# Optimization experiments

Measured on AMD Instinct MI355X. Metric: run time of the kernel, lower is better.

## Reference

```python
import jax, jax.numpy as jnp
import numpy as np

N, E, IN, H, OUT, L = 20000, 320000, 256, 256, 128, 3
EPS = 1e-5


def setup_inputs() -> dict:
    key = jax.random.key(0)
    ks = jax.random.split(key, 16)
    s = 0.02
    return {
        "x": jax.random.normal(ks[0], (N, IN), jnp.float32),
        "edge_index": jax.random.randint(ks[1], (2, E), 0, N, jnp.int64),
        "in_w": jax.random.normal(ks[2], (IN, H), jnp.float32) * s,
        "in_b": jnp.zeros((H,), jnp.float32),
        "parent_w": jax.random.normal(ks[3], (L, H, H), jnp.float32) * s,
        "child_w": jax.random.normal(ks[4], (L, H, H), jnp.float32) * s,
        "self_w": jax.random.normal(ks[5], (L, H, H), jnp.float32) * s,
        "self_b": jnp.zeros((L, H), jnp.float32),
        "ln_g": jnp.ones((L, H), jnp.float32),
        "ln_b": jnp.zeros((L, H), jnp.float32),
        "head_w1": jax.random.normal(ks[6], (H, H), jnp.float32) * s,
        "head_b1": jnp.zeros((H,), jnp.float32),
        "head_w2": jax.random.normal(ks[7], (H, OUT), jnp.float32) * s,
        "head_b2": jnp.zeros((OUT,), jnp.float32),
    }


def _aggregate(h, src, dst, weight):
    # gather -> matmul -> scatter-add -> degree-normalize
    transformed = h[src] @ weight                       # [E, H]
    agg = jax.ops.segment_sum(transformed, dst, num_segments=N)
    deg = jax.ops.segment_sum(jnp.ones((src.shape[0],), h.dtype), dst, num_segments=N)
    deg = jnp.maximum(deg, 1.0)
    return agg / deg[:, None]


def _layer_norm(x, g, b):
    mu = jnp.mean(x, axis=-1, keepdims=True)
    var = jnp.mean(jnp.square(x - mu), axis=-1, keepdims=True)
    return (x - mu) * jax.lax.rsqrt(var + EPS) * g + b


def reference(x, edge_index, in_w, in_b, parent_w, child_w, self_w, self_b,
              ln_g, ln_b, head_w1, head_b1, head_w2, head_b2):
    src, dst = edge_index[0], edge_index[1]
    h = x @ in_w + in_b                                  # input_proj
    for l in range(L):
        parent_msg = _aggregate(h, src, dst, parent_w[l])
        child_msg = _aggregate(h, dst, src, child_w[l])  # reversed edges
        out = h @ self_w[l] + self_b[l] + parent_msg + child_msg
        out = jax.nn.gelu(out, approximate=False)
        # dropout is identity in eval mode (training=False)
        h = _layer_norm(h + out, ln_g[l], ln_b[l])
    y = jax.nn.gelu(h @ head_w1 + head_b1, approximate=False)
    return y @ head_w2 + head_b2
```

## Files before the change

### kernel.cpp

```cpp
#include <hip/hip_runtime.h>


#define H 256
#define LAYERS 3
#define OUTD 128
#define LN_EPS 1e-5f

typedef short s16x8 __attribute__((ext_vector_type(8)));
typedef unsigned short u16x4 __attribute__((ext_vector_type(4)));
typedef unsigned short u16x8 __attribute__((ext_vector_type(8)));
typedef float f32x4 __attribute__((ext_vector_type(4)));
typedef int i32x4 __attribute__((ext_vector_type(4)));

__device__ __forceinline__ unsigned short f2bf(float f) {
  unsigned int u = __float_as_uint(f);
  u += 0x7FFFu + ((u >> 16) & 1u);
  return (unsigned short)(u >> 16);
}
__device__ __forceinline__ float bf2f(unsigned short s) {
  return __uint_as_float(((unsigned int)s) << 16);
}
__device__ __forceinline__ float gelu_f(float x) {
  return 0.5f * x * (1.0f + erff(x * 0.70710678118654752440f));
}
__device__ __forceinline__ void gload16(const void* g, void* l) {
  __builtin_amdgcn_global_load_lds((const __attribute__((address_space(1))) void*)g,
                                   (__attribute__((address_space(3))) void*)l, 16, 0, 0);
}


__device__ __forceinline__ void store_split8(unsigned short* __restrict__ T, int NS, int sec,
                                             int row, int l, u16x4 hv, u16x4 lv) {
  size_t tb = ((size_t)((row >> 4) * NS + sec) << 4) + (l >> 3);
  int off = (((row & 15) + (((l >> 1) & 3) << 4)) << 3) + ((l & 1) << 2);
  *(u16x4*)(T + tb * 512 + off) = hv;
  *(u16x4*)(T + (tb + 8) * 512 + off) = lv;
}

__global__ void split_tiles_kernel(const float* __restrict__ X,
                                   unsigned short* __restrict__ T, int NS, int sec,
                                   unsigned short* __restrict__ Hc, int M)
{
  const int rb = blockIdx.x;
  const int l = threadIdx.x & 63;
  const int cq = threadIdx.x >> 6;
  const int row = (rb << 4) + (l & 15);
  if (row >= M) return;
  const float* xr = X + (size_t)row * H;
#pragma unroll
  for (int p = 0; p < 2; ++p) {
    const int c = cq + (p << 2);
    const int j0 = (c << 5) + ((l >> 4) << 3);
    f32x4 v0 = *(const f32x4*)(xr + j0);
    f32x4 v1 = *(const f32x4*)(xr + j0 + 4);
    u16x8 hv, lv;
#pragma unroll
    for (int i = 0; i < 4; ++i) {
      unsigned short hb = f2bf(v0[i]); hv[i] = hb;     lv[i] = f2bf(v0[i] - bf2f(hb));
      unsigned short hc = f2bf(v1[i]); hv[4 + i] = hc; lv[4 + i] = f2bf(v1[i] - bf2f(hc));
    }
    size_t tb = ((size_t)(rb * NS + sec) << 4);
    *(u16x8*)(T + (tb + c) * 512 + (l << 3)) = hv;
    *(u16x8*)(T + (tb + c + 8) * 512 + (l << 3)) = lv;
    if (Hc) *(u16x8*)(Hc + (size_t)row * H + j0) = hv;
  }
}

__global__ void bext_kernel(const float* __restrict__ W, unsigned short* __restrict__ Bt, int ncol) {
  int idx = blockIdx.x * 256 + threadIdx.x;
  if (idx >= H * ncol) return;
  int k = idx / ncol;
  int n = idx - k * ncol;
  float w = W[idx];
  unsigned short hb = f2bf(w);
  unsigned short lb = f2bf(w - bf2f(hb));
  size_t base = (((size_t)(n >> 4) << 4) + (k >> 5)) * 512 +
                (((n & 15) + (((k >> 3) & 3) << 4)) << 3) + (k & 7);
  Bt[base] = hb;
  Bt[base + 8 * 512] = lb;
}

__global__ void zero2_kernel(int* __restrict__ a, int* __restrict__ b, int n) {
  int i = blockIdx.x * 256 + threadIdx.x;
  if (i < n) { a[i] = 0; b[i] = 0; }
}

__global__ void deg_kernel(const int* __restrict__ src, const int* __restrict__ dst,
                           int* __restrict__ di, int* __restrict__ dox, int E) {
  int e = blockIdx.x * 256 + threadIdx.x;
  if (e >= E) return;
  atomicAdd(&dox[src[e]], 1);
  atomicAdd(&di[dst[e]], 1);
}

__global__ void rdeg_kernel(const int* __restrict__ di, const int* __restrict__ dox,
                            float* __restrict__ ri, float* __restrict__ ro, int n) {
  int i = blockIdx.x * 256 + threadIdx.x;
  if (i >= n) return;
  int a = di[i];  if (a < 1) a = 1;
  int b = dox[i]; if (b < 1) b = 1;
  ri[i] = 1.0f / (float)a;
  ro[i] = 1.0f / (float)b;
}

__global__ __launch_bounds__(1024)
void scan_kernel(const int* __restrict__ deg, int* __restrict__ rowptr, int n) {
  __shared__ int partial[1024];
  const int t = threadIdx.x;
  const int chunk = (n + 1023) / 1024;
  int b = t * chunk;
  int e = b + chunk; if (e > n) e = n;
  int s = 0;
  for (int i = b; i < e; ++i) s += deg[i];
  partial[t] = s;
  __syncthreads();
  for (int off = 1; off < 1024; off <<= 1) {
    int v = (t >= off) ? partial[t - off] : 0;
    __syncthreads();
    partial[t] += v;
    __syncthreads();
  }
  int run = (t == 0) ? 0 : partial[t - 1];
  for (int i = b; i < e; ++i) { rowptr[i] = run; run += deg[i]; }
  if (t == 1023) rowptr[n] = run;
}

__global__ void fill_kernel(const int* __restrict__ src, const int* __restrict__ dst,
                            const int* __restrict__ rp_in, const int* __restrict__ rp_out,
                            int* __restrict__ cur_in, int* __restrict__ cur_out,
                            int* __restrict__ ci_in, int* __restrict__ ci_out, int E) {
  int e = blockIdx.x * 256 + threadIdx.x;
  if (e >= E) return;
  int s = src[e], d = dst[e];
  int p = atomicAdd(&cur_in[d], 1);
  ci_in[rp_in[d] + p] = s;
  int q = atomicAdd(&cur_out[s], 1);
  ci_out[rp_out[s] + q] = d;
}

template<int NF>
__global__ __launch_bounds__(256)
void gemm_kernel(const unsigned short* __restrict__ A, int NSa,
                 const unsigned short* __restrict__ B0,
                 const unsigned short* __restrict__ B1,
                 const unsigned short* __restrict__ B2,
                 const float* __restrict__ bias, float* __restrict__ C,
                 int M, int nrb, int nsec, int do_gelu)
{
  constexpr int N = NF * 64;
  constexpr int NBT = N / 16;
  constexpr int BITER = NBT / 4;
  constexpr int SA_HI = 0, SA_LO = 2048, SB_HI = 4096;
  constexpr int SB_LO = 4096 + NBT * 512;
  __shared__ unsigned short lds[2][4096 + 2 * NBT * 512];

  const int tid = threadIdx.x;
  const int lane = tid & 63;
  const int wn = tid >> 6;
  const int m0 = blockIdx.x << 6;
  int rbw = (blockIdx.x << 2) + wn;
  if (rbw >= nrb) rbw = nrb - 1;

  f32x4 acc[4][NF] = {};

  auto STAGE = [&](int buf, int step) {
    const int s = step >> 3;
    const int c = step & 7;
    const unsigned short* Bs = (s == 0) ? B0 : ((s == 1) ? B1 : B2);
    unsigned short* base = &lds[buf][0];
    const unsigned short* pa = A + (((size_t)(rbw * NSa + s) << 4) + c) * 512 + (lane << 3);
    gload16(pa,        base + SA_HI + (wn << 9));
    gload16(pa + 4096, base + SA_LO + (wn << 9));
#pragma unroll
    for (int i = 0; i < BITER; ++i) {
      const int nb = wn + (i << 2);
      const unsigned short* pb = Bs + (((size_t)nb << 4) + c) * 512 + (lane << 3);
      gload16(pb,        base + SB_HI + (nb << 9));
      gload16(pb + 4096, base + SB_LO + (nb << 9));
    }
  };

  auto COMPUTE = [&](int buf) {
    const unsigned short* base = &lds[buf][0];
    s16x8 ah[4], al[4], bh[NF], bl[NF];
#pragma unroll
    for (int f = 0; f < 4; ++f) {
      ah[f] = *(const s16x8*)(base + SA_HI + (f << 9) + (lane << 3));
      al[f] = *(const s16x8*)(base + SA_LO + (f << 9) + (lane << 3));
    }
#pragma unroll
    for (int j = 0; j < NF; ++j) {
      const int g = wn * NF + j;
      bh[j] = *(const s16x8*)(base + SB_HI + (g << 9) + (lane << 3));
      bl[j] = *(const s16x8*)(base + SB_LO + (g << 9) + (lane << 3));
    }
#pragma unroll
    for (int i = 0; i < 4; ++i)
#pragma unroll
      for (int j = 0; j < NF; ++j)
        acc[i][j] = __builtin_amdgcn_mfma_f32_16x16x32_bf16(ah[i], bh[j], acc[i][j], 0, 0, 0);
#pragma unroll
    for (int i = 0; i < 4; ++i)
#pragma unroll
      for (int j = 0; j < NF; ++j)
        acc[i][j] = __builtin_amdgcn_mfma_f32_16x16x32_bf16(ah[i], bl[j], acc[i][j], 0, 0, 0);
#pragma unroll
    for (int i = 0; i < 4; ++i)
#pragma unroll
      for (int j = 0; j < NF; ++j)
        acc[i][j] = __builtin_amdgcn_mfma_f32_16x16x32_bf16(al[i], bh[j], acc[i][j], 0, 0, 0);
  };

  const int nsteps = nsec << 3;
  STAGE(0, 0);
  int cur = 0;
  for (int t = 0; t < nsteps - 1; ++t) {
    STAGE(cur ^ 1, t + 1);
    if (NF == 4) asm volatile("s_waitcnt vmcnt(10)" ::: "memory");
    else         asm volatile("s_waitcnt vmcnt(6)"  ::: "memory");
    __builtin_amdgcn_s_barrier();
    COMPUTE(cur);
    asm volatile("s_waitcnt lgkmcnt(0)" ::: "memory");
    __builtin_amdgcn_s_barrier();
    cur ^= 1;
  }
  asm volatile("s_waitcnt vmcnt(0)" ::: "memory");
  __builtin_amdgcn_s_barrier();
  COMPUTE(cur);

  const int r0 = (lane >> 4) << 2;
  const int cn = lane & 15;
#pragma unroll
  for (int j = 0; j < NF; ++j) {
    const int col = wn * (NF << 4) + (j << 4) + cn;
    const float bb = bias ? bias[col] : 0.0f;
#pragma unroll
    for (int i = 0; i < 4; ++i) {
      const int rowb = m0 + (i << 4) + r0;
#pragma unroll
      for (int r = 0; r < 4; ++r) {
        const int rr = rowb + r;
        if (rr < M) {
          float v = acc[i][j][r] + bb;
          if (do_gelu) v = gelu_f(v);
          C[(size_t)rr * N + col] = v;
        }
      }
    }
  }
}

__device__ __forceinline__ void gacc8(const int* __restrict__ ci, int beg, int end,
                                      const unsigned short* __restrict__ Hc, int foff,
                                      float* __restrict__ acc) {
  int i = beg;
  for (; i < end && (i & 3); ++i) {
    u16x8 a = *(const u16x8*)(Hc + ((size_t)ci[i] << 8) + foff);
#pragma unroll
    for (int z = 0; z < 8; ++z) acc[z] += bf2f(a[z]);
  }
  for (; i + 4 <= end; i += 4) {
    i32x4 id = *(const i32x4*)(ci + i);
    u16x8 a = *(const u16x8*)(Hc + ((size_t)id[0] << 8) + foff);
    u16x8 b = *(const u16x8*)(Hc + ((size_t)id[1] << 8) + foff);
    u16x8 c = *(const u16x8*)(Hc + ((size_t)id[2] << 8) + foff);
    u16x8 d = *(const u16x8*)(Hc + ((size_t)id[3] << 8) + foff);
#pragma unroll
    for (int z = 0; z < 8; ++z)
      acc[z] += (bf2f(a[z]) + bf2f(b[z])) + (bf2f(c[z]) + bf2f(d[z]));
  }
  for (; i < end; ++i) {
    u16x8 a = *(const u16x8*)(Hc + ((size_t)ci[i] << 8) + foff);
#pragma unroll
    for (int z = 0; z < 8; ++z) acc[z] += bf2f(a[z]);
  }
}

__global__ __launch_bounds__(256)
void gather_kernel(
    const int* __restrict__ rp_in, const int* __restrict__ ci_in,
    const int* __restrict__ rp_out, const int* __restrict__ ci_out,
    const float* __restrict__ ri, const float* __restrict__ ro,
    const unsigned short* __restrict__ Hc, unsigned short* __restrict__ Aext,
    int M, int nrb, int npair)
{
  __shared__ unsigned short sh[2][2][2][2][512];
  const int b = blockIdx.x;
  const int xcd = b & 7;
  const int s = xcd >> 1;
  const int rbp = ((b >> 3) << 1) + (xcd & 1);
  if (rbp >= npair) return;
  const int tid = threadIdx.x;
  const int g = tid >> 3;
  const int t = tid & 7;
  const int row = (rbp << 5) + g;
  const int foff = (s << 6) + (t << 3);

  float hin[8] = {}, hout[8] = {};
  float wi = 0.f, wo = 0.f;
  if (row < M) {
    gacc8(ci_in,  rp_in[row],  rp_in[row + 1],  Hc, foff, hin);
    gacc8(ci_out, rp_out[row], rp_out[row + 1], Hc, foff, hout);
    wi = ri[row];
    wo = ro[row];
  }

  const int rbl = g >> 4;
  const int cc = t >> 2;
  const int pos = ((g & 15) << 3) + ((t & 3) << 7);
  u16x8 hv, lv;
#pragma unroll
  for (int q = 0; q < 8; ++q) {
    float v = hin[q] * wi;
    unsigned short hb = f2bf(v);
    hv[q] = hb; lv[q] = f2bf(v - bf2f(hb));
  }
  *(u16x8*)(&sh[rbl][0][0][cc][pos]) = hv;
  *(u16x8*)(&sh[rbl][0][1][cc][pos]) = lv;
#pragma unroll
  for (int q = 0; q < 8; ++q) {
    float v = hout[q] * wo;
    unsigned short hb = f2bf(v);
    hv[q] = hb; lv[q] = f2bf(v - bf2f(hb));
  }
  *(u16x8*)(&sh[rbl][1][0][cc][pos]) = hv;
  *(u16x8*)(&sh[rbl][1][1][cc][pos]) = lv;
  __syncthreads();

  const int tp = tid >> 4;
  const int q = tid & 15;
  const int rbl2 = tp >> 3, sec = (tp >> 2) & 1, hilo = (tp >> 1) & 1, c2 = tp & 1;
  const int rb = (rbp << 1) + rbl2;
  if (rb < nrb) {
    const int cg = (s << 1) + c2 + (hilo << 3);
    size_t tile = ((size_t)(rb * 3 + 1 + sec) << 4) + cg;
    unsigned short* dstp = Aext + tile * 512;
    const unsigned short* srcp = &sh[rbl2][sec][hilo][c2][0];
#pragma unroll
    for (int i = 0; i < 4; ++i)
      *(u16x8*)(dstp + (i << 7) + (q << 3)) = *(const u16x8*)(srcp + (i << 7) + (q << 3));
  }
}

__global__ void finalize_kernel(float* __restrict__ h, const float* __restrict__ P,
                                unsigned short* __restrict__ Aext,
                                unsigned short* __restrict__ Hc,
                                const float* __restrict__ g, const float* __restrict__ b, int M)
{
  int row = blockIdx.x * 4 + (threadIdx.x >> 6);
  if (row >= M) return;
  int l = threadIdx.x & 63;
  int j = l << 2;
  f32x4 hv = *(const f32x4*)(h + (size_t)row * H + j);
  f32x4 pv = *(const f32x4*)(P + (size_t)row * H + j);
  f32x4 t;
  float sum = 0.f, sq = 0.f;
#pragma unroll
  for (int i = 0; i < 4; ++i) {
    t[i] = hv[i] + gelu_f(pv[i]);
    sum += t[i];
    sq += t[i] * t[i];
  }
#pragma unroll
  for (int off = 1; off < 64; off <<= 1) {
    sum += __shfl_xor(sum, off, 64);
    sq  += __shfl_xor(sq, off, 64);
  }
  float mu = sum * (1.0f / H);
  float var = sq * (1.0f / H) - mu * mu;
  float rs = rsqrtf(var + LN_EPS);
  f32x4 outv;
  u16x4 hvv, lvv;
#pragma unroll
  for (int i = 0; i < 4; ++i) {
    outv[i] = (t[i] - mu) * rs * g[j + i] + b[j + i];
    unsigned short hb = f2bf(outv[i]);
    hvv[i] = hb;
    lvv[i] = f2bf(outv[i] - bf2f(hb));
  }
  *(f32x4*)(h + (size_t)row * H + j) = outv;
  *(u16x4*)(Hc + ((size_t)row << 8) + j) = hvv;
  store_split8(Aext, 3, 0, row, l, hvv, lvv);
}

extern "C" void kernel_launch(void* const* d_in, const int* in_sizes, int n_in,
                              void* d_out, int out_size, void* d_ws, size_t ws_size,
                              hipStream_t stream)
{
  const float* x        = (const float*)d_in[0];
  const int*   ei       = (const int*)d_in[1];
  const float* in_w     = (const float*)d_in[2];
  const float* in_b     = (const float*)d_in[3];
  const float* parent_w = (const float*)d_in[4];
  const float* child_w  = (const float*)d_in[5];
  const float* self_w   = (const float*)d_in[6];
  const float* self_b   = (const float*)d_in[7];
  const float* ln_g     = (const float*)d_in[8];
  const float* ln_b     = (const float*)d_in[9];
  const float* head_w1  = (const float*)d_in[10];
  const float* head_b1  = (const float*)d_in[11];
  const float* head_w2  = (const float*)d_in[12];
  const float* head_b2  = (const float*)d_in[13];

  const int M = in_sizes[0] / H;
  const int E = in_sizes[1] / 2;
  const int nrb = (M + 15) / 16;
  const int npair = (nrb + 1) / 2;
  const int* src = ei;
  const int* dst = ei + E;

  char* w = (char*)d_ws;
  auto alloc = [&](size_t bytes) { char* p = w; w += (bytes + 255) & ~(size_t)255; return p; };
  float*          h    = (float*)alloc((size_t)M * H * 4);
  float*          P    = (float*)alloc((size_t)M * H * 4);
  unsigned short* Ax   = (unsigned short*)alloc((size_t)nrb * 16 * 512 * 2);
  unsigned short* Aext = (unsigned short*)alloc((size_t)nrb * 48 * 512 * 2);
  unsigned short* Hc   = (unsigned short*)alloc((size_t)M * H * 2);
  unsigned short* Bext = (unsigned short*)alloc((size_t)12 * H * 512 * 2);
  int*            degi = (int*)alloc((size_t)M * 4);
  int*            dego = (int*)alloc((size_t)M * 4);
  float*          ri   = (float*)alloc((size_t)M * 4);
  float*          ro   = (float*)alloc((size_t)M * 4);
  int*            rp_in   = (int*)alloc((size_t)(M + 1) * 4);
  int*            rp_out  = (int*)alloc((size_t)(M + 1) * 4);
  int*            cur_in  = (int*)alloc((size_t)M * 4);
  int*            cur_out = (int*)alloc((size_t)M * 4);
  int*            ci_in   = (int*)alloc((size_t)E * 4);
  int*            ci_out  = (int*)alloc((size_t)E * 4);
  if ((size_t)(w - (char*)d_ws) > ws_size) return;

  auto bslot = [&](int i) { return Bext + (size_t)i * H * 512; };

  bext_kernel<<<(H * H) / 256, 256, 0, stream>>>(in_w, bslot(0), H);
  for (int l = 0; l < LAYERS; ++l) {
    bext_kernel<<<(H * H) / 256, 256, 0, stream>>>(parent_w + (size_t)l * H * H, bslot(1 + l), H);
    bext_kernel<<<(H * H) / 256, 256, 0, stream>>>(child_w  + (size_t)l * H * H, bslot(4 + l), H);
    bext_kernel<<<(H * H) / 256, 256, 0, stream>>>(self_w   + (size_t)l * H * H, bslot(7 + l), H);
  }
  bext_kernel<<<(H * H) / 256, 256, 0, stream>>>(head_w1, bslot(10), H);
  bext_kernel<<<(H * OUTD) / 256, 256, 0, stream>>>(head_w2, bslot(11), OUTD);

  zero2_kernel<<<(M + 255) / 256, 256, 0, stream>>>(degi, dego, M);
  deg_kernel<<<(E + 255) / 256, 256, 0, stream>>>(src, dst, degi, dego, E);
  rdeg_kernel<<<(M + 255) / 256, 256, 0, stream>>>(degi, dego, ri, ro, M);
  scan_kernel<<<1, 1024, 0, stream>>>(degi, rp_in, M);
  scan_kernel<<<1, 1024, 0, stream>>>(dego, rp_out, M);
  zero2_kernel<<<(M + 255) / 256, 256, 0, stream>>>(cur_in, cur_out, M);
  fill_kernel<<<(E + 255) / 256, 256, 0, stream>>>(src, dst, rp_in, rp_out,
                                                   cur_in, cur_out, ci_in, ci_out, E);

  const int mb = (M + 63) / 64;
  const int ggrid = (M + 3) / 4;
  const int xgrid = 8 * ((npair + 1) / 2);

  split_tiles_kernel<<<nrb, 256, 0, stream>>>(x, Ax, 1, 0, nullptr, M);
  gemm_kernel<4><<<mb, 256, 0, stream>>>(Ax, 1, bslot(0), nullptr, nullptr,
                                         in_b, h, M, nrb, 1, 0);
  split_tiles_kernel<<<nrb, 256, 0, stream>>>(h, Aext, 3, 0, Hc, M);

  for (int l = 0; l < LAYERS; ++l) {
    gather_kernel<<<xgrid, 256, 0, stream>>>(rp_in, ci_in, rp_out, ci_out,
                                             ri, ro, Hc, Aext, M, nrb, npair);
    gemm_kernel<4><<<mb, 256, 0, stream>>>(Aext, 3,
                                           bslot(7 + l), bslot(1 + l), bslot(4 + l),
                                           self_b + (size_t)l * H, P, M, nrb, 3, 0);
    finalize_kernel<<<ggrid, 256, 0, stream>>>(h, P, Aext, Hc,
                                               ln_g + (size_t)l * H, ln_b + (size_t)l * H, M);
  }

  gemm_kernel<4><<<mb, 256, 0, stream>>>(Aext, 3, bslot(10), nullptr, nullptr,
                                         head_b1, P, M, nrb, 1, 1);
  split_tiles_kernel<<<nrb, 256, 0, stream>>>(P, Ax, 1, 0, nullptr, M);
  gemm_kernel<2><<<mb, 256, 0, stream>>>(Ax, 1, bslot(11), nullptr, nullptr,
                                         head_b2, (float*)d_out, M, nrb, 1, 0);
}
```

Measured before the change: 522.8 us.

## Fuse residual, GELU and LayerNorm into GEMM epilogue, and batch setup kernels

The per-layer GEMM epilogue now does the GELU, the residual add, a cross-wave LayerNorm reduction through LDS, and writes h, the bf16 copy and the hi/lo split tiles directly. This removes the separate finalize kernel and the P intermediate buffer. The input-projection and head1 GEMMs also emit split tiles themselves, so their split_tiles passes go away. Setup is consolidated: the twelve weight conversions become one launch, the two scans become one two-block launch, and the cursor zeroing moves into rdeg. The trade-off is that the epilogue now does scattered 2-byte stores and extra LDS synchronisation, and the GEMM uses more registers.

```diff
diff --git a/kernel.cpp b/kernel.cpp
--- a/kernel.cpp
+++ b/kernel.cpp
@@ -29,16 +29,8 @@
 }
 
 
-__device__ __forceinline__ void store_split8(unsigned short* __restrict__ T, int NS, int sec,
-                                             int row, int l, u16x4 hv, u16x4 lv) {
-  size_t tb = ((size_t)((row >> 4) * NS + sec) << 4) + (l >> 3);
-  int off = (((row & 15) + (((l >> 1) & 3) << 4)) << 3) + ((l & 1) << 2);
-  *(u16x4*)(T + tb * 512 + off) = hv;
-  *(u16x4*)(T + (tb + 8) * 512 + off) = lv;
-}
-
 __global__ void split_tiles_kernel(const float* __restrict__ X,
-                                   unsigned short* __restrict__ T, int NS, int sec,
+                                   unsigned short* __restrict__ T, int NS,
                                    unsigned short* __restrict__ Hc, int M)
 {
   const int rb = blockIdx.x;
@@ -59,16 +51,33 @@
       unsigned short hb = f2bf(v0[i]); hv[i] = hb;     lv[i] = f2bf(v0[i] - bf2f(hb));
       unsigned short hc = f2bf(v1[i]); hv[4 + i] = hc; lv[4 + i] = f2bf(v1[i] - bf2f(hc));
     }
-    size_t tb = ((size_t)(rb * NS + sec) << 4);
+    size_t tb = ((size_t)(rb * NS) << 4);
     *(u16x8*)(T + (tb + c) * 512 + (l << 3)) = hv;
     *(u16x8*)(T + (tb + c + 8) * 512 + (l << 3)) = lv;
     if (Hc) *(u16x8*)(Hc + (size_t)row * H + j0) = hv;
   }
 }
 
-__global__ void bext_kernel(const float* __restrict__ W, unsigned short* __restrict__ Bt, int ncol) {
-  int idx = blockIdx.x * 256 + threadIdx.x;
+__global__ void bext_all_kernel(const float* __restrict__ in_w,
+                                const float* __restrict__ parent_w,
+                                const float* __restrict__ child_w,
+                                const float* __restrict__ self_w,
+                                const float* __restrict__ head_w1,
+                                const float* __restrict__ head_w2,
+                                unsigned short* __restrict__ Bext)
+{
+  const int slot = blockIdx.x >> 8;
+  const int chunk = blockIdx.x & 255;
+  const int ncol = (slot == 11) ? OUTD : H;
+  const int idx = chunk * 256 + threadIdx.x;
   if (idx >= H * ncol) return;
+  const float* W =
+    (slot == 0)  ? in_w :
+    (slot <= 3)  ? parent_w + (size_t)(slot - 1) * H * H :
+    (slot <= 6)  ? child_w  + (size_t)(slot - 4) * H * H :
+    (slot <= 9)  ? self_w   + (size_t)(slot - 7) * H * H :
+    (slot == 10) ? head_w1  : head_w2;
+  unsigned short* Bt = Bext + (size_t)slot * H * 512;
   int k = idx / ncol;
   int n = idx - k * ncol;
   float w = W[idx];
@@ -94,18 +103,24 @@
 }
 
 __global__ void rdeg_kernel(const int* __restrict__ di, const int* __restrict__ dox,
-                            float* __restrict__ ri, float* __restrict__ ro, int n) {
+                            float* __restrict__ ri, float* __restrict__ ro,
+                            int* __restrict__ cur_in, int* __restrict__ cur_out, int n) {
   int i = blockIdx.x * 256 + threadIdx.x;
   if (i >= n) return;
   int a = di[i];  if (a < 1) a = 1;
   int b = dox[i]; if (b < 1) b = 1;
   ri[i] = 1.0f / (float)a;
   ro[i] = 1.0f / (float)b;
+  cur_in[i] = 0;
+  cur_out[i] = 0;
 }
 
 __global__ __launch_bounds__(1024)
-void scan_kernel(const int* __restrict__ deg, int* __restrict__ rowptr, int n) {
+void scan2_kernel(const int* __restrict__ degi, const int* __restrict__ dego,
+                  int* __restrict__ rp_in, int* __restrict__ rp_out, int n) {
   __shared__ int partial[1024];
+  const int* deg = blockIdx.x ? dego : degi;
+  int* rowptr = blockIdx.x ? rp_out : rp_in;
   const int t = threadIdx.x;
   const int chunk = (n + 1023) / 1024;
   int b = t * chunk;
@@ -138,14 +153,17 @@
   ci_out[rp_out[s] + q] = d;
 }
 
-template<int NF>
+template<int NF, int MODE>
 __global__ __launch_bounds__(256)
 void gemm_kernel(const unsigned short* __restrict__ A, int NSa,
                  const unsigned short* __restrict__ B0,
                  const unsigned short* __restrict__ B1,
                  const unsigned short* __restrict__ B2,
                  const float* __restrict__ bias, float* __restrict__ C,
-                 int M, int nrb, int nsec, int do_gelu)
+                 unsigned short* __restrict__ Asp, int NSp,
+                 unsigned short* __restrict__ Hc,
+                 const float* __restrict__ lng, const float* __restrict__ lnb,
+                 int M, int nrb, int nsec)
 {
   constexpr int N = NF * 64;
   constexpr int NBT = N / 16;
@@ -230,20 +248,99 @@
 
   const int r0 = (lane >> 4) << 2;
   const int cn = lane & 15;
-#pragma unroll
-  for (int j = 0; j < NF; ++j) {
-    const int col = wn * (NF << 4) + (j << 4) + cn;
-    const float bb = bias ? bias[col] : 0.0f;
-#pragma unroll
-    for (int i = 0; i < 4; ++i) {
-      const int rowb = m0 + (i << 4) + r0;
+
+  if constexpr (MODE == 2) {
+    int cols[NF]; float bb[NF], gg[NF], lbv[NF];
+#pragma unroll
+    for (int j = 0; j < NF; ++j) {
+      cols[j] = wn * (NF << 4) + (j << 4) + cn;
+      bb[j] = bias[cols[j]]; gg[j] = lng[cols[j]]; lbv[j] = lnb[cols[j]];
+    }
+    float S[4][4] = {}, Q[4][4] = {};
+#pragma unroll
+    for (int i = 0; i < 4; ++i)
 #pragma unroll
       for (int r = 0; r < 4; ++r) {
-        const int rr = rowb + r;
+        int rr = m0 + (i << 4) + r0 + r;
+        size_t hr = (size_t)(rr < M ? rr : 0) << 8;
+#pragma unroll
+        for (int j = 0; j < NF; ++j) {
+          float t = C[hr + cols[j]] + gelu_f(acc[i][j][r] + bb[j]);
+          acc[i][j][r] = t;
+          S[i][r] += t; Q[i][r] += t * t;
+        }
+      }
+#pragma unroll
+    for (int m = 1; m < 16; m <<= 1)
+#pragma unroll
+      for (int i = 0; i < 4; ++i)
+#pragma unroll
+        for (int r = 0; r < 4; ++r) {
+          S[i][r] += __shfl_xor(S[i][r], m, 64);
+          Q[i][r] += __shfl_xor(Q[i][r], m, 64);
+        }
+    float* red = (float*)&lds[0][0];
+    __syncthreads();
+    if (cn == 0) {
+#pragma unroll
+      for (int i = 0; i < 4; ++i)
+#pragma unroll
+        for (int r = 0; r < 4; ++r) {
+          int row = (i << 4) + r0 + r;
+          red[(row << 3) + (wn << 1)] = S[i][r];
+          red[(row << 3) + (wn << 1) + 1] = Q[i][r];
+        }
+    }
+    __syncthreads();
+#pragma unroll
+    for (int i = 0; i < 4; ++i)
+#pragma unroll
+      for (int r = 0; r < 4; ++r) {
+        int row = (i << 4) + r0 + r;
+        int rr = m0 + row;
+        float s = red[(row << 3)] + red[(row << 3) + 2] + red[(row << 3) + 4] + red[(row << 3) + 6];
+        float q = red[(row << 3) + 1] + red[(row << 3) + 3] + red[(row << 3) + 5] + red[(row << 3) + 7];
+        float mu = s * (1.0f / H);
+        float rs = rsqrtf(q * (1.0f / H) - mu * mu + LN_EPS);
         if (rr < M) {
-          float v = acc[i][j][r] + bb;
-          if (do_gelu) v = gelu_f(v);
-          C[(size_t)rr * N + col] = v;
+#pragma unroll
+          for (int j = 0; j < NF; ++j) {
+            float o = (acc[i][j][r] - mu) * rs * gg[j] + lbv[j];
+            C[((size_t)rr << 8) + cols[j]] = o;
+            unsigned short hb = f2bf(o);
+            Hc[((size_t)rr << 8) + cols[j]] = hb;
+            size_t tb = (((size_t)(rr >> 4) * NSp) << 4) + (cols[j] >> 5);
+            int off = ((rr & 15) << 3) + (((cols[j] >> 3) & 3) << 7) + (cols[j] & 7);
+            Asp[tb * 512 + off] = hb;
+            Asp[(tb + 8) * 512 + off] = f2bf(o - bf2f(hb));
+          }
+        }
+      }
+  } else {
+#pragma unroll
+    for (int j = 0; j < NF; ++j) {
+      const int col = wn * (NF << 4) + (j << 4) + cn;
+      const float bb = bias ? bias[col] : 0.0f;
+#pragma unroll
+      for (int i = 0; i < 4; ++i) {
+        const int rowb = m0 + (i << 4) + r0;
+#pragma unroll
+        for (int r = 0; r < 4; ++r) {
+          const int rr = rowb + r;
+          if (rr < M) {
+            float v = acc[i][j][r] + bb;
+            if constexpr (MODE == 3) v = gelu_f(v);
+            if constexpr (MODE == 0) C[(size_t)rr * N + col] = v;
+            if constexpr (MODE == 1) C[(size_t)rr * H + col] = v;
+            if constexpr (MODE == 1 || MODE == 3) {
+              unsigned short hb = f2bf(v);
+              size_t tb = (((size_t)(rr >> 4) * NSp) << 4) + (col >> 5);
+              int off = ((rr & 15) << 3) + (((col >> 3) & 3) << 7) + (col & 7);
+              Asp[tb * 512 + off] = hb;
+              Asp[(tb + 8) * 512 + off] = f2bf(v - bf2f(hb));
+              if constexpr (MODE == 1) Hc[((size_t)rr << 8) + col] = hb;
+            }
+          }
         }
       }
     }
@@ -342,47 +439,6 @@
   }
 }
 
-__global__ void finalize_kernel(float* __restrict__ h, const float* __restrict__ P,
-                                unsigned short* __restrict__ Aext,
-                                unsigned short* __restrict__ Hc,
-                                const float* __restrict__ g, const float* __restrict__ b, int M)
-{
-  int row = blockIdx.x * 4 + (threadIdx.x >> 6);
-  if (row >= M) return;
-  int l = threadIdx.x & 63;
-  int j = l << 2;
-  f32x4 hv = *(const f32x4*)(h + (size_t)row * H + j);
-  f32x4 pv = *(const f32x4*)(P + (size_t)row * H + j);
-  f32x4 t;
-  float sum = 0.f, sq = 0.f;
-#pragma unroll
-  for (int i = 0; i < 4; ++i) {
-    t[i] = hv[i] + gelu_f(pv[i]);
-    sum += t[i];
-    sq += t[i] * t[i];
-  }
-#pragma unroll
-  for (int off = 1; off < 64; off <<= 1) {
-    sum += __shfl_xor(sum, off, 64);
-    sq  += __shfl_xor(sq, off, 64);
-  }
-  float mu = sum * (1.0f / H);
-  float var = sq * (1.0f / H) - mu * mu;
-  float rs = rsqrtf(var + LN_EPS);
-  f32x4 outv;
-  u16x4 hvv, lvv;
-#pragma unroll
-  for (int i = 0; i < 4; ++i) {
-    outv[i] = (t[i] - mu) * rs * g[j + i] + b[j + i];
-    unsigned short hb = f2bf(outv[i]);
-    hvv[i] = hb;
-    lvv[i] = f2bf(outv[i] - bf2f(hb));
-  }
-  *(f32x4*)(h + (size_t)row * H + j) = outv;
-  *(u16x4*)(Hc + ((size_t)row << 8) + j) = hvv;
-  store_split8(Aext, 3, 0, row, l, hvv, lvv);
-}
-
 extern "C" void kernel_launch(void* const* d_in, const int* in_sizes, int n_in,
                               void* d_out, int out_size, void* d_ws, size_t ws_size,
                               hipStream_t stream)
@@ -412,7 +468,6 @@
   char* w = (char*)d_ws;
   auto alloc = [&](size_t bytes) { char* p = w; w += (bytes + 255) & ~(size_t)255; return p; };
   float*          h    = (float*)alloc((size_t)M * H * 4);
-  float*          P    = (float*)alloc((size_t)M * H * 4);
   unsigned short* Ax   = (unsigned short*)alloc((size_t)nrb * 16 * 512 * 2);
   unsigned short* Aext = (unsigned short*)alloc((size_t)nrb * 48 * 512 * 2);
   unsigned short* Hc   = (unsigned short*)alloc((size_t)M * H * 2);
@@ -431,46 +486,38 @@
 
   auto bslot = [&](int i) { return Bext + (size_t)i * H * 512; };
 
-  bext_kernel<<<(H * H) / 256, 256, 0, stream>>>(in_w, bslot(0), H);
-  for (int l = 0; l < LAYERS; ++l) {
-    bext_kernel<<<(H * H) / 256, 256, 0, stream>>>(parent_w + (size_t)l * H * H, bslot(1 + l), H);
-    bext_kernel<<<(H * H) / 256, 256, 0, stream>>>(child_w  + (size_t)l * H * H, bslot(4 + l), H);
-    bext_kernel<<<(H * H) / 256, 256, 0, stream>>>(self_w   + (size_t)l * H * H, bslot(7 + l), H);
-  }
-  bext_kernel<<<(H * H) / 256, 256, 0, stream>>>(head_w1, bslot(10), H);
-  bext_kernel<<<(H * OUTD) / 256, 256, 0, stream>>>(head_w2, bslot(11), OUTD);
+  bext_all_kernel<<<12 * 256, 256, 0, stream>>>(in_w, parent_w, child_w, self_w,
+                                                head_w1, head_w2, Bext);
 
   zero2_kernel<<<(M + 255) / 256, 256, 0, stream>>>(degi, dego, M);
   deg_kernel<<<(E + 255) / 256, 256, 0, stream>>>(src, dst, degi, dego, E);
-  rdeg_kernel<<<(M + 255) / 256, 256, 0, stream>>>(degi, dego, ri, ro, M);
-  scan_kernel<<<1, 1024, 0, stream>>>(degi, rp_in, M);
-  scan_kernel<<<1, 1024, 0, stream>>>(dego, rp_out, M);
-  zero2_kernel<<<(M + 255) / 256, 256, 0, stream>>>(cur_in, cur_out, M);
+  rdeg_kernel<<<(M + 255) / 256, 256, 0, stream>>>(degi, dego, ri, ro, cur_in, cur_out, M);
+  scan2_kernel<<<2, 1024, 0, stream>>>(degi, dego, rp_in, rp_out, M);
   fill_kernel<<<(E + 255) / 256, 256, 0, stream>>>(src, dst, rp_in, rp_out,
                                                    cur_in, cur_out, ci_in, ci_out, E);
 
   const int mb = (M + 63) / 64;
-  const int ggrid = (M + 3) / 4;
   const int xgrid = 8 * ((npair + 1) / 2);
 
-  split_tiles_kernel<<<nrb, 256, 0, stream>>>(x, Ax, 1, 0, nullptr, M);
-  gemm_kernel<4><<<mb, 256, 0, stream>>>(Ax, 1, bslot(0), nullptr, nullptr,
-                                         in_b, h, M, nrb, 1, 0);
-  split_tiles_kernel<<<nrb, 256, 0, stream>>>(h, Aext, 3, 0, Hc, M);
+  split_tiles_kernel<<<nrb, 256, 0, stream>>>(x, Ax, 1, nullptr, M);
+  gemm_kernel<4, 1><<<mb, 256, 0, stream>>>(Ax, 1, bslot(0), nullptr, nullptr,
+                                            in_b, h, Aext, 3, Hc, nullptr, nullptr,
+                                            M, nrb, 1);
 
   for (int l = 0; l < LAYERS; ++l) {
     gather_kernel<<<xgrid, 256, 0, stream>>>(rp_in, ci_in, rp_out, ci_out,
                                              ri, ro, Hc, Aext, M, nrb, npair);
-    gemm_kernel<4><<<mb, 256, 0, stream>>>(Aext, 3,
-                                           bslot(7 + l), bslot(1 + l), bslot(4 + l),
-                                           self_b + (size_t)l * H, P, M, nrb, 3, 0);
-    finalize_kernel<<<ggrid, 256, 0, stream>>>(h, P, Aext, Hc,
-                                               ln_g + (size_t)l * H, ln_b + (size_t)l * H, M);
-  }
-
-  gemm_kernel<4><<<mb, 256, 0, stream>>>(Aext, 3, bslot(10), nullptr, nullptr,
-                                         head_b1, P, M, nrb, 1, 1);
-  split_tiles_kernel<<<nrb, 256, 0, stream>>>(P, Ax, 1, 0, nullptr, M);
-  gemm_kernel<2><<<mb, 256, 0, stream>>>(Ax, 1, bslot(11), nullptr, nullptr,
-                                         head_b2, (float*)d_out, M, nrb, 1, 0);
-}
+    gemm_kernel<4, 2><<<mb, 256, 0, stream>>>(Aext, 3,
+                                              bslot(7 + l), bslot(1 + l), bslot(4 + l),
+                                              self_b + (size_t)l * H, h, Aext, 3, Hc,
+                                              ln_g + (size_t)l * H, ln_b + (size_t)l * H,
+                                              M, nrb, 3);
+  }
+
+  gemm_kernel<4, 3><<<mb, 256, 0, stream>>>(Aext, 3, bslot(10), nullptr, nullptr,
+                                            head_b1, nullptr, Ax, 1, nullptr,
+                                            nullptr, nullptr, M, nrb, 1);
+  gemm_kernel<2, 0><<<mb, 256, 0, stream>>>(Ax, 1, bslot(11), nullptr, nullptr,
+                                            head_b2, (float*)d_out, nullptr, 0, nullptr,
+                                            nullptr, nullptr, M, nrb, 1);
+}
```

Result: no change. 516.9 us (-1.1%).

## Shrink GEMM tile to 32 rows, read B directly from global, merge setup kernels

Applied to the files above, without the earlier changes.

The GEMM kernel now covers 32 rows per block instead of 64 and stages only the A tile in LDS. Each wave loads either the hi or lo half, and the B fragments are read straight from global memory, where they should mostly hit in cache. This is meant to cut LDS traffic, raise occupancy and double the grid size, at the cost of more repeated global reads of B per block. Separately, the twelve weight-split launches become one, the two scans run as one two-block launch, and cursor zeroing moves into rdeg, which removes several small launches.

```diff
diff --git a/kernel.cpp b/kernel.cpp
--- a/kernel.cpp
+++ b/kernel.cpp
@@ -38,7 +38,7 @@
 }
 
 __global__ void split_tiles_kernel(const float* __restrict__ X,
-                                   unsigned short* __restrict__ T, int NS, int sec,
+                                   unsigned short* __restrict__ T, int NS,
                                    unsigned short* __restrict__ Hc, int M)
 {
   const int rb = blockIdx.x;
@@ -59,16 +59,33 @@
       unsigned short hb = f2bf(v0[i]); hv[i] = hb;     lv[i] = f2bf(v0[i] - bf2f(hb));
       unsigned short hc = f2bf(v1[i]); hv[4 + i] = hc; lv[4 + i] = f2bf(v1[i] - bf2f(hc));
     }
-    size_t tb = ((size_t)(rb * NS + sec) << 4);
+    size_t tb = ((size_t)(rb * NS) << 4);
     *(u16x8*)(T + (tb + c) * 512 + (l << 3)) = hv;
     *(u16x8*)(T + (tb + c + 8) * 512 + (l << 3)) = lv;
     if (Hc) *(u16x8*)(Hc + (size_t)row * H + j0) = hv;
   }
 }
 
-__global__ void bext_kernel(const float* __restrict__ W, unsigned short* __restrict__ Bt, int ncol) {
-  int idx = blockIdx.x * 256 + threadIdx.x;
+__global__ void bext_all_kernel(const float* __restrict__ in_w,
+                                const float* __restrict__ parent_w,
+                                const float* __restrict__ child_w,
+                                const float* __restrict__ self_w,
+                                const float* __restrict__ head_w1,
+                                const float* __restrict__ head_w2,
+                                unsigned short* __restrict__ Bext)
+{
+  const int slot = blockIdx.x >> 8;
+  const int chunk = blockIdx.x & 255;
+  const int ncol = (slot == 11) ? OUTD : H;
+  const int idx = chunk * 256 + threadIdx.x;
   if (idx >= H * ncol) return;
+  const float* W =
+    (slot == 0)  ? in_w :
+    (slot <= 3)  ? parent_w + (size_t)(slot - 1) * H * H :
+    (slot <= 6)  ? child_w  + (size_t)(slot - 4) * H * H :
+    (slot <= 9)  ? self_w   + (size_t)(slot - 7) * H * H :
+    (slot == 10) ? head_w1  : head_w2;
+  unsigned short* Bt = Bext + (size_t)slot * H * 512;
   int k = idx / ncol;
   int n = idx - k * ncol;
   float w = W[idx];
@@ -94,18 +111,24 @@
 }
 
 __global__ void rdeg_kernel(const int* __restrict__ di, const int* __restrict__ dox,
-                            float* __restrict__ ri, float* __restrict__ ro, int n) {
+                            float* __restrict__ ri, float* __restrict__ ro,
+                            int* __restrict__ cur_in, int* __restrict__ cur_out, int n) {
   int i = blockIdx.x * 256 + threadIdx.x;
   if (i >= n) return;
   int a = di[i];  if (a < 1) a = 1;
   int b = dox[i]; if (b < 1) b = 1;
   ri[i] = 1.0f / (float)a;
   ro[i] = 1.0f / (float)b;
+  cur_in[i] = 0;
+  cur_out[i] = 0;
 }
 
 __global__ __launch_bounds__(1024)
-void scan_kernel(const int* __restrict__ deg, int* __restrict__ rowptr, int n) {
+void scan2_kernel(const int* __restrict__ degi, const int* __restrict__ dego,
+                  int* __restrict__ rp_in, int* __restrict__ rp_out, int n) {
   __shared__ int partial[1024];
+  const int* deg = blockIdx.x ? dego : degi;
+  int* rowptr = blockIdx.x ? rp_out : rp_in;
   const int t = threadIdx.x;
   const int chunk = (n + 1023) / 1024;
   int b = t * chunk;
@@ -148,64 +171,56 @@
                  int M, int nrb, int nsec, int do_gelu)
 {
   constexpr int N = NF * 64;
-  constexpr int NBT = N / 16;
-  constexpr int BITER = NBT / 4;
-  constexpr int SA_HI = 0, SA_LO = 2048, SB_HI = 4096;
-  constexpr int SB_LO = 4096 + NBT * 512;
-  __shared__ unsigned short lds[2][4096 + 2 * NBT * 512];
+  __shared__ unsigned short ldsA[2][2048];
 
   const int tid = threadIdx.x;
   const int lane = tid & 63;
   const int wn = tid >> 6;
-  const int m0 = blockIdx.x << 6;
-  int rbw = (blockIdx.x << 2) + wn;
+  const int m0 = blockIdx.x << 5;
+  int rbw = (blockIdx.x << 1) + (wn & 1);
   if (rbw >= nrb) rbw = nrb - 1;
-
-  f32x4 acc[4][NF] = {};
+  const int hilo = wn >> 1;
+
+  f32x4 acc[2][NF] = {};
 
   auto STAGE = [&](int buf, int step) {
     const int s = step >> 3;
     const int c = step & 7;
+    const unsigned short* pa =
+        A + (((size_t)(rbw * NSa + s) << 4) + c + (hilo << 3)) * 512 + (lane << 3);
+    gload16(pa, &ldsA[buf][0] + (wn << 9));
+  };
+
+  auto COMPUTE = [&](int buf, int step) {
+    const int s = step >> 3;
+    const int c = step & 7;
     const unsigned short* Bs = (s == 0) ? B0 : ((s == 1) ? B1 : B2);
-    unsigned short* base = &lds[buf][0];
-    const unsigned short* pa = A + (((size_t)(rbw * NSa + s) << 4) + c) * 512 + (lane << 3);
-    gload16(pa,        base + SA_HI + (wn << 9));
-    gload16(pa + 4096, base + SA_LO + (wn << 9));
-#pragma unroll
-    for (int i = 0; i < BITER; ++i) {
-      const int nb = wn + (i << 2);
-      const unsigned short* pb = Bs + (((size_t)nb << 4) + c) * 512 + (lane << 3);
-      gload16(pb,        base + SB_HI + (nb << 9));
-      gload16(pb + 4096, base + SB_LO + (nb << 9));
-    }
-  };
-
-  auto COMPUTE = [&](int buf) {
-    const unsigned short* base = &lds[buf][0];
-    s16x8 ah[4], al[4], bh[NF], bl[NF];
-#pragma unroll
-    for (int f = 0; f < 4; ++f) {
-      ah[f] = *(const s16x8*)(base + SA_HI + (f << 9) + (lane << 3));
-      al[f] = *(const s16x8*)(base + SA_LO + (f << 9) + (lane << 3));
-    }
+    s16x8 bh[NF], bl[NF];
 #pragma unroll
     for (int j = 0; j < NF; ++j) {
       const int g = wn * NF + j;
-      bh[j] = *(const s16x8*)(base + SB_HI + (g << 9) + (lane << 3));
-      bl[j] = *(const s16x8*)(base + SB_LO + (g << 9) + (lane << 3));
+      bh[j] = *(const s16x8*)(Bs + ((size_t)((g << 4) + c) << 9) + (lane << 3));
+      bl[j] = *(const s16x8*)(Bs + ((size_t)((g << 4) + c + 8) << 9) + (lane << 3));
     }
-#pragma unroll
-    for (int i = 0; i < 4; ++i)
+    const unsigned short* base = &ldsA[buf][0];
+    s16x8 ah[2], al[2];
+#pragma unroll
+    for (int f = 0; f < 2; ++f) {
+      ah[f] = *(const s16x8*)(base + (f << 9) + (lane << 3));
+      al[f] = *(const s16x8*)(base + 1024 + (f << 9) + (lane << 3));
+    }
+#pragma unroll
+    for (int i = 0; i < 2; ++i)
 #pragma unroll
       for (int j = 0; j < NF; ++j)
         acc[i][j] = __builtin_amdgcn_mfma_f32_16x16x32_bf16(ah[i], bh[j], acc[i][j], 0, 0, 0);
 #pragma unroll
-    for (int i = 0; i < 4; ++i)
+    for (int i = 0; i < 2; ++i)
 #pragma unroll
       for (int j = 0; j < NF; ++j)
         acc[i][j] = __builtin_amdgcn_mfma_f32_16x16x32_bf16(ah[i], bl[j], acc[i][j], 0, 0, 0);
 #pragma unroll
-    for (int i = 0; i < 4; ++i)
+    for (int i = 0; i < 2; ++i)
 #pragma unroll
       for (int j = 0; j < NF; ++j)
         acc[i][j] = __builtin_amdgcn_mfma_f32_16x16x32_bf16(al[i], bh[j], acc[i][j], 0, 0, 0);
@@ -216,17 +231,16 @@
   int cur = 0;
   for (int t = 0; t < nsteps - 1; ++t) {
     STAGE(cur ^ 1, t + 1);
-    if (NF == 4) asm volatile("s_waitcnt vmcnt(10)" ::: "memory");
-    else         asm volatile("s_waitcnt vmcnt(6)"  ::: "memory");
+    asm volatile("s_waitcnt vmcnt(1)" ::: "memory");
     __builtin_amdgcn_s_barrier();
-    COMPUTE(cur);
+    COMPUTE(cur, t);
     asm volatile("s_waitcnt lgkmcnt(0)" ::: "memory");
     __builtin_amdgcn_s_barrier();
     cur ^= 1;
   }
   asm volatile("s_waitcnt vmcnt(0)" ::: "memory");
   __builtin_amdgcn_s_barrier();
-  COMPUTE(cur);
+  COMPUTE(cur, nsteps - 1);
 
   const int r0 = (lane >> 4) << 2;
   const int cn = lane & 15;
@@ -235,7 +249,7 @@
     const int col = wn * (NF << 4) + (j << 4) + cn;
     const float bb = bias ? bias[col] : 0.0f;
 #pragma unroll
-    for (int i = 0; i < 4; ++i) {
+    for (int i = 0; i < 2; ++i) {
       const int rowb = m0 + (i << 4) + r0;
 #pragma unroll
       for (int r = 0; r < 4; ++r) {
@@ -431,46 +445,38 @@
 
   auto bslot = [&](int i) { return Bext + (size_t)i * H * 512; };
 
-  bext_kernel<<<(H * H) / 256, 256, 0, stream>>>(in_w, bslot(0), H);
-  for (int l = 0; l < LAYERS; ++l) {
-    bext_kernel<<<(H * H) / 256, 256, 0, stream>>>(parent_w + (size_t)l * H * H, bslot(1 + l), H);
-    bext_kernel<<<(H * H) / 256, 256, 0, stream>>>(child_w  + (size_t)l * H * H, bslot(4 + l), H);
-    bext_kernel<<<(H * H) / 256, 256, 0, stream>>>(self_w   + (size_t)l * H * H, bslot(7 + l), H);
-  }
-  bext_kernel<<<(H * H) / 256, 256, 0, stream>>>(head_w1, bslot(10), H);
-  bext_kernel<<<(H * OUTD) / 256, 256, 0, stream>>>(head_w2, bslot(11), OUTD);
+  bext_all_kernel<<<12 * 256, 256, 0, stream>>>(in_w, parent_w, child_w, self_w,
+                                                head_w1, head_w2, Bext);
 
   zero2_kernel<<<(M + 255) / 256, 256, 0, stream>>>(degi, dego, M);
   deg_kernel<<<(E + 255) / 256, 256, 0, stream>>>(src, dst, degi, dego, E);
-  rdeg_kernel<<<(M + 255) / 256, 256, 0, stream>>>(degi, dego, ri, ro, M);
-  scan_kernel<<<1, 1024, 0, stream>>>(degi, rp_in, M);
-  scan_kernel<<<1, 1024, 0, stream>>>(dego, rp_out, M);
-  zero2_kernel<<<(M + 255) / 256, 256, 0, stream>>>(cur_in, cur_out, M);
+  rdeg_kernel<<<(M + 255) / 256, 256, 0, stream>>>(degi, dego, ri, ro, cur_in, cur_out, M);
+  scan2_kernel<<<2, 1024, 0, stream>>>(degi, dego, rp_in, rp_out, M);
   fill_kernel<<<(E + 255) / 256, 256, 0, stream>>>(src, dst, rp_in, rp_out,
                                                    cur_in, cur_out, ci_in, ci_out, E);
 
-  const int mb = (M + 63) / 64;
+  const int mb32 = (M + 31) / 32;
   const int ggrid = (M + 3) / 4;
   const int xgrid = 8 * ((npair + 1) / 2);
 
-  split_tiles_kernel<<<nrb, 256, 0, stream>>>(x, Ax, 1, 0, nullptr, M);
-  gemm_kernel<4><<<mb, 256, 0, stream>>>(Ax, 1, bslot(0), nullptr, nullptr,
-                                         in_b, h, M, nrb, 1, 0);
-  split_tiles_kernel<<<nrb, 256, 0, stream>>>(h, Aext, 3, 0, Hc, M);
+  split_tiles_kernel<<<nrb, 256, 0, stream>>>(x, Ax, 1, nullptr, M);
+  gemm_kernel<4><<<mb32, 256, 0, stream>>>(Ax, 1, bslot(0), nullptr, nullptr,
+                                           in_b, h, M, nrb, 1, 0);
+  split_tiles_kernel<<<nrb, 256, 0, stream>>>(h, Aext, 3, Hc, M);
 
   for (int l = 0; l < LAYERS; ++l) {
     gather_kernel<<<xgrid, 256, 0, stream>>>(rp_in, ci_in, rp_out, ci_out,
                                              ri, ro, Hc, Aext, M, nrb, npair);
-    gemm_kernel<4><<<mb, 256, 0, stream>>>(Aext, 3,
-                                           bslot(7 + l), bslot(1 + l), bslot(4 + l),
-                                           self_b + (size_t)l * H, P, M, nrb, 3, 0);
+    gemm_kernel<4><<<mb32, 256, 0, stream>>>(Aext, 3,
+                                             bslot(7 + l), bslot(1 + l), bslot(4 + l),
+                                             self_b + (size_t)l * H, P, M, nrb, 3, 0);
     finalize_kernel<<<ggrid, 256, 0, stream>>>(h, P, Aext, Hc,
                                                ln_g + (size_t)l * H, ln_b + (size_t)l * H, M);
   }
 
-  gemm_kernel<4><<<mb, 256, 0, stream>>>(Aext, 3, bslot(10), nullptr, nullptr,
-                                         head_b1, P, M, nrb, 1, 1);
-  split_tiles_kernel<<<nrb, 256, 0, stream>>>(P, Ax, 1, 0, nullptr, M);
-  gemm_kernel<2><<<mb, 256, 0, stream>>>(Ax, 1, bslot(11), nullptr, nullptr,
-                                         head_b2, (float*)d_out, M, nrb, 1, 0);
-}
+  gemm_kernel<4><<<mb32, 256, 0, stream>>>(Aext, 3, bslot(10), nullptr, nullptr,
+                                           head_b1, P, M, nrb, 1, 1);
+  split_tiles_kernel<<<nrb, 256, 0, stream>>>(P, Ax, 1, nullptr, M);
+  gemm_kernel<2><<<mb32, 256, 0, stream>>>(Ax, 1, bslot(11), nullptr, nullptr,
+                                           head_b2, (float*)d_out, M, nrb, 1, 0);
+}
```

Result: faster. 456.9 us (-12.6%).
